# Performance work log

Hardware: AMD Instinct MI355X
Metric: run time of the kernel (lower is better)

Reference implementation:

```python
import jax, jax.numpy as jnp
import numpy as np

B, C, H, W = 128, 512, 8, 64   # batch, featrue_layers, feature-map H/W
HID, EMB = 512, 512            # hidden_dim_de, embedding_size


def setup_inputs() -> dict:
    key = jax.random.key(0)
    ks = jax.random.split(key, 8)
    s_lin = 1.0 / np.sqrt(HID)
    s_conv = 1.0 / np.sqrt(C * 9)
    s_att = 1.0 / np.sqrt(EMB)
    return {
        "conv_f": jax.random.normal(ks[0], (B, C, H, W), jnp.float32),
        "h": jax.random.normal(ks[1], (B, HID), jnp.float32),
        "W_h": jax.random.uniform(ks[2], (EMB, HID), jnp.float32, -s_lin, s_lin),
        "b_h": jax.random.uniform(ks[3], (EMB,), jnp.float32, -s_lin, s_lin),
        "K_conv": jax.random.uniform(ks[4], (EMB, C, 3, 3), jnp.float32, -s_conv, s_conv),
        "b_conv": jax.random.uniform(ks[5], (EMB,), jnp.float32, -s_conv, s_conv),
        "w_att": jax.random.uniform(ks[6], (1, EMB), jnp.float32, -s_att, s_att),
        "b_att": jax.random.uniform(ks[7], (1,), jnp.float32, -s_att, s_att),
    }


def reference(conv_f, h, W_h, b_h, K_conv, b_conv, w_att, b_att):
    b, c, hh, ww = conv_f.shape
    L = hh * ww
    # g_em = Linear(h): [B, EMB], broadcast over L positions
    g_em = h @ W_h.T + b_h                                   # [B, EMB]
    # x_em = Conv2d(conv_f): [B, EMB, H, W] -> [B, L, EMB]
    x_em = jax.lax.conv_general_dilated(
        conv_f, K_conv, window_strides=(1, 1), padding="SAME",
        dimension_numbers=("NCHW", "OIHW", "NCHW"))
    x_em = x_em + b_conv[None, :, None, None]
    x_em = x_em.reshape(b, -1, L).transpose(0, 2, 1)         # [B, L, EMB]
    # additive attention scores (dropout = identity in eval mode)
    feat = jnp.tanh(x_em + g_em[:, None, :])                 # [B, L, EMB]
    e = feat @ w_att[0] + b_att[0]                           # [B, L]
    alpha = jax.nn.softmax(e, axis=-1)                       # [B, L]
    # weighted sum over positions of the ORIGINAL features
    org = conv_f.reshape(b, c, L)                            # [B, C, L]
    att_out = jnp.einsum("bl,bcl->bc", alpha, org)           # [B, C]
    return att_out, alpha
```

## Files before the change

kernel.cpp:

```cpp
#include <hip/hip_runtime.h>
#include <hip/hip_bf16.h>
#include <stdint.h>

#define B_ 128
#define C_ 512
#define H_ 8
#define W_ 64
#define L_ 512
#define EMB_ 512
#define HID_ 512
#define M_ 65536
#define PH 10
#define PW 66
#define PADSZ (B_*PH*PW*C_)
#define BT_SZ (9*EMB_*C_)
#define GEM_SZ (B_*EMB_)

typedef __attribute__((ext_vector_type(8))) short short8;
typedef __attribute__((ext_vector_type(4))) float f32x4;

__device__ __forceinline__ void gload16(const void* g, void* l) {
    __builtin_amdgcn_global_load_lds(
        (const __attribute__((address_space(1))) unsigned int*)g,
        (__attribute__((address_space(3))) unsigned int*)l, 16, 0, 0);
}

__device__ __forceinline__ float fast_tanh(float x) {
    float e = __expf(2.0f * fabsf(x));
    float r = 1.0f - __fdividef(2.0f, e + 1.0f);
    return copysignf(r, x);
}

__global__ __launch_bounds__(256) void k_pad(const float* __restrict__ cf,
                                             __hip_bfloat16* __restrict__ pad) {
    int bid = blockIdx.x, t = threadIdx.x;
    int b = bid >> 3, y = bid & 7;
    for (int cc = 0; cc < 2; ++cc) {
        int c = cc * 256 + t;
        const float* src = cf + ((size_t)(b * C_ + c) * H_ + y) * W_;
        __hip_bfloat16* dst = pad + ((size_t)(b * PH + y + 1) * PW + 1) * C_ + c;
#pragma unroll
        for (int x = 0; x < W_; ++x)
            dst[(size_t)x * C_] = __float2bfloat16(src[x]);
    }
}

__global__ __launch_bounds__(256) void k_wt(const float* __restrict__ kc,
                                            __hip_bfloat16* __restrict__ bt) {
    int e = blockIdx.x, t = threadIdx.x;
    for (int cc = 0; cc < 2; ++cc) {
        int c = cc * 256 + t;
        const float* src = kc + (size_t)(e * C_ + c) * 9;
#pragma unroll
        for (int tap = 0; tap < 9; ++tap)
            bt[(size_t)tap * EMB_ * C_ + e * C_ + c] = __float2bfloat16(src[tap]);
    }
}

__global__ __launch_bounds__(256) void k_gem(const float* __restrict__ h,
                                             const float* __restrict__ Wh,
                                             const float* __restrict__ bh,
                                             float* __restrict__ gem) {
    int b = blockIdx.x, t = threadIdx.x;
    __shared__ float hs[HID_];
    hs[t] = h[b * HID_ + t];
    hs[t + 256] = h[b * HID_ + t + 256];
    __syncthreads();
    for (int e = t; e < EMB_; e += 256) {
        float acc = bh[e];
        const float4* wr = (const float4*)(Wh + (size_t)e * HID_);
#pragma unroll 4
        for (int k4 = 0; k4 < HID_ / 4; ++k4) {
            float4 w = wr[k4];
            const float* hp = &hs[k4 * 4];
            acc += w.x * hp[0] + w.y * hp[1] + w.z * hp[2] + w.w * hp[3];
        }
        gem[b * EMB_ + e] = acc;
    }
}

#define MFMA16(a,b,c) __builtin_amdgcn_mfma_f32_16x16x32_bf16(a,b,c,0,0,0)

__global__ __launch_bounds__(512, 2) void k_conv(const __hip_bfloat16* __restrict__ pad,
                                                 const __hip_bfloat16* __restrict__ bt,
                                                 const float* __restrict__ gem,
                                                 const float* __restrict__ bconv,
                                                 const float* __restrict__ watt,
                                                 float* __restrict__ sp) {
    __shared__ __align__(16) char lds[131072];
    const int tid = threadIdx.x;
    const int lane = tid & 63, wid = tid >> 6;
    const int wm = wid >> 2, wn = wid & 3;
    int bid0 = blockIdx.x;
    int bid = (bid0 & 7) * 64 + (bid0 >> 3);
    const int tile_m = bid >> 1, tile_n = bid & 1;
    const int b = tile_m >> 1;

    int gA[4], gB[4];
#pragma unroll
    for (int i = 0; i < 4; ++i) {
        int s = i * 8192 + tid * 16;
        int row = s >> 7;
        int clocal = ((s & 127) ^ ((row & 7) << 4)) >> 1;
        int m = tile_m * 256 + row;
        int y = (m >> 6) & 7;
        int x = m & 63;
        gA[i] = ((b * PH + y) * PW + x) * C_ + clocal;
        int e = tile_n * 256 + row;
        gB[i] = e * C_ + clocal;
    }
    const int lsw = wid * 1024;

    const int la = lane & 15, lg = lane >> 4;
    const int xorv = (la & 7) << 4;
    const int cb0 = (lg * 16) ^ xorv;
    const int cb1 = (64 + lg * 16) ^ xorv;

    f32x4 acc[8][4];
#pragma unroll
    for (int i = 0; i < 8; ++i)
#pragma unroll
        for (int j = 0; j < 4; ++j) acc[i][j] = (f32x4){0.f, 0.f, 0.f, 0.f};

#define STAGE_A(i, nb, aofs) gload16(pad + gA[i] + (aofs), lds + (nb)*65536 + (i)*8192 + lsw)
#define STAGE_B(i, nb, bofs) gload16(bt + gB[i] + (bofs), lds + (nb)*65536 + 32768 + (i)*8192 + lsw)

    STAGE_A(0, 0, 0); STAGE_A(1, 0, 0); STAGE_A(2, 0, 0); STAGE_A(3, 0, 0);
    STAGE_B(0, 0, 0); STAGE_B(1, 0, 0); STAGE_B(2, 0, 0); STAGE_B(3, 0, 0);

    for (int kt = 0; kt < 72; ++kt) {
        const int cur = kt & 1, nb = cur ^ 1;
        const char* bufA = lds + cur * 65536;
        const char* bufB = bufA + 32768;
        const int ktn = (kt < 71) ? kt + 1 : 71;
        const int tapn = ktn >> 3;
        const int dyn_ = tapn / 3, dxn_ = tapn - dyn_ * 3;
        const int aofsn = (dyn_ * PW + dxn_) * C_ + ((ktn & 7) << 6);
        const int bofsn = tapn * (EMB_ * C_) + ((ktn & 7) << 6);

        short8 af[8], bq0, bq1;
        STAGE_A(0, nb, aofsn); STAGE_A(1, nb, aofsn);
        asm volatile("s_waitcnt vmcnt(2)" ::: "memory");
        __builtin_amdgcn_s_barrier();
#pragma unroll
        for (int fm = 0; fm < 8; ++fm)
            af[fm] = *(const short8*)(bufA + (wm * 128 + fm * 16 + la) * 128 + cb0);
        bq0 = *(const short8*)(bufB + (wn * 64 + la) * 128 + cb0);
        bq1 = *(const short8*)(bufB + (wn * 64 + 16 + la) * 128 + cb0);
        __builtin_amdgcn_s_setprio(1);
#pragma unroll
        for (int fm = 0; fm < 8; ++fm) {
            acc[fm][0] = MFMA16(af[fm], bq0, acc[fm][0]);
            acc[fm][1] = MFMA16(af[fm], bq1, acc[fm][1]);
        }
        __builtin_amdgcn_s_setprio(0);
        STAGE_A(2, nb, aofsn); STAGE_A(3, nb, aofsn);
        bq0 = *(const short8*)(bufB + (wn * 64 + 32 + la) * 128 + cb0);
        bq1 = *(const short8*)(bufB + (wn * 64 + 48 + la) * 128 + cb0);
        __builtin_amdgcn_s_setprio(1);
#pragma unroll
        for (int fm = 0; fm < 8; ++fm) {
            acc[fm][2] = MFMA16(af[fm], bq0, acc[fm][2]);
            acc[fm][3] = MFMA16(af[fm], bq1, acc[fm][3]);
        }
        __builtin_amdgcn_s_setprio(0);
        STAGE_B(0, nb, bofsn); STAGE_B(1, nb, bofsn);
#pragma unroll
        for (int fm = 0; fm < 8; ++fm)
            af[fm] = *(const short8*)(bufA + (wm * 128 + fm * 16 + la) * 128 + cb1);
        bq0 = *(const short8*)(bufB + (wn * 64 + la) * 128 + cb1);
        bq1 = *(const short8*)(bufB + (wn * 64 + 16 + la) * 128 + cb1);
        __builtin_amdgcn_s_setprio(1);
#pragma unroll
        for (int fm = 0; fm < 8; ++fm) {
            acc[fm][0] = MFMA16(af[fm], bq0, acc[fm][0]);
            acc[fm][1] = MFMA16(af[fm], bq1, acc[fm][1]);
        }
        __builtin_amdgcn_s_setprio(0);
        STAGE_B(2, nb, bofsn); STAGE_B(3, nb, bofsn);
        bq0 = *(const short8*)(bufB + (wn * 64 + 32 + la) * 128 + cb1);
        bq1 = *(const short8*)(bufB + (wn * 64 + 48 + la) * 128 + cb1);
        __builtin_amdgcn_s_setprio(1);
#pragma unroll
        for (int fm = 0; fm < 8; ++fm) {
            acc[fm][2] = MFMA16(af[fm], bq0, acc[fm][2]);
            acc[fm][3] = MFMA16(af[fm], bq1, acc[fm][3]);
        }
        __builtin_amdgcn_s_setprio(0);
        __builtin_amdgcn_s_barrier();
    }
    asm volatile("s_waitcnt vmcnt(0)" ::: "memory");

    const int part = tile_n * 4 + wn;
    float addv[4], wv[4];
#pragma unroll
    for (int fn = 0; fn < 4; ++fn) {
        int e = tile_n * 256 + wn * 64 + fn * 16 + la;
        addv[fn] = bconv[e] + gem[b * EMB_ + e];
        wv[fn] = watt[e];
    }
#pragma unroll
    for (int fm = 0; fm < 8; ++fm) {
        float sj[4] = {0.f, 0.f, 0.f, 0.f};
#pragma unroll
        for (int fn = 0; fn < 4; ++fn)
#pragma unroll
            for (int j = 0; j < 4; ++j)
                sj[j] += fast_tanh(acc[fm][fn][j] + addv[fn]) * wv[fn];
#pragma unroll
        for (int mask = 1; mask < 16; mask <<= 1)
#pragma unroll
            for (int j = 0; j < 4; ++j)
                sj[j] += __shfl_xor(sj[j], mask, 64);
        if (la == 0) {
            int mrow = tile_m * 256 + wm * 128 + fm * 16 + lg * 4;
            *(float4*)(sp + (size_t)part * M_ + mrow) =
                make_float4(sj[0], sj[1], sj[2], sj[3]);
        }
    }
}

__global__ __launch_bounds__(512) void k_softmax(const float* __restrict__ sp,
                                                 const float* __restrict__ batt,
                                                 float* __restrict__ alpha) {
    int b = blockIdx.x, t = threadIdx.x;
    float s = batt[0];
#pragma unroll
    for (int p = 0; p < 8; ++p) s += sp[(size_t)p * M_ + b * L_ + t];
    int lane = t & 63, wid = t >> 6;
    __shared__ float red[8];
    float m = s;
#pragma unroll
    for (int mask = 1; mask < 64; mask <<= 1) m = fmaxf(m, __shfl_xor(m, mask, 64));
    if (lane == 0) red[wid] = m;
    __syncthreads();
    float M = red[0];
#pragma unroll
    for (int i = 1; i < 8; ++i) M = fmaxf(M, red[i]);
    float ev = __expf(s - M);
    float sum = ev;
#pragma unroll
    for (int mask = 1; mask < 64; mask <<= 1) sum += __shfl_xor(sum, mask, 64);
    __syncthreads();
    if (lane == 0) red[wid] = sum;
    __syncthreads();
    float S = 0.f;
#pragma unroll
    for (int i = 0; i < 8; ++i) S += red[i];
    alpha[b * L_ + t] = ev / S;
}

__global__ __launch_bounds__(256) void k_att(const float* __restrict__ cf,
                                             const float* __restrict__ alpha,
                                             float* __restrict__ att) {
    int bid = blockIdx.x;
    int b = bid >> 7, cg = bid & 127;
    int t = threadIdx.x, lane = t & 63, wid = t >> 6;
    int c = cg * 4 + wid;
    const float4* xr = (const float4*)(cf + (size_t)(b * C_ + c) * L_);
    const float4* ar = (const float4*)(alpha + b * L_);
    float acc = 0.f;
#pragma unroll
    for (int it = 0; it < 2; ++it) {
        float4 xv = xr[it * 64 + lane];
        float4 av = ar[it * 64 + lane];
        acc += xv.x * av.x + xv.y * av.y + xv.z * av.z + xv.w * av.w;
    }
#pragma unroll
    for (int mask = 1; mask < 64; mask <<= 1) acc += __shfl_xor(acc, mask, 64);
    if (lane == 0) att[b * C_ + c] = acc;
}

extern "C" void kernel_launch(void* const* d_in, const int* in_sizes, int n_in,
                              void* d_out, int out_size, void* d_ws, size_t ws_size,
                              hipStream_t stream) {
    const float* conv_f = (const float*)d_in[0];
    const float* h      = (const float*)d_in[1];
    const float* W_h    = (const float*)d_in[2];
    const float* b_h    = (const float*)d_in[3];
    const float* K_conv = (const float*)d_in[4];
    const float* b_conv = (const float*)d_in[5];
    const float* w_att  = (const float*)d_in[6];
    const float* b_att  = (const float*)d_in[7];
    float* out = (float*)d_out;

    char* ws = (char*)d_ws;
    __hip_bfloat16* pad = (__hip_bfloat16*)ws;
    __hip_bfloat16* bt  = (__hip_bfloat16*)(ws + (size_t)PADSZ * 2);
    float* gem = (float*)(ws + (size_t)PADSZ * 2 + (size_t)BT_SZ * 2);
    float* sp  = gem + GEM_SZ;

    hipMemsetAsync(pad, 0, (size_t)PADSZ * 2, stream);
    k_pad<<<B_ * H_, 256, 0, stream>>>(conv_f, pad);
    k_wt<<<EMB_, 256, 0, stream>>>(K_conv, bt);
    k_gem<<<B_, 256, 0, stream>>>(h, W_h, b_h, gem);
    k_conv<<<512, 512, 0, stream>>>(pad, bt, gem, b_conv, w_att, sp);
    float* alpha = out + B_ * C_;
    k_softmax<<<B_, 512, 0, stream>>>(sp, b_att, alpha);
    k_att<<<B_ * C_ / 4, 256, 0, stream>>>(conv_f, alpha, out);
}
```

Baseline: 527.7 us.

## Switch conv GEMM to 32x32 MFMA, fuse pad zeroing, parallelize gem

The conv GEMM inner loop now uses 32x32x16 bf16 MFMA tiles, which cuts LDS fragment reads per MFMA. All next-tile global-to-LDS loads are issued at the start of each iteration rather than interleaved with compute. The full-buffer memset of the padded input is replaced by zeroing only the border rows and columns inside the pad kernel. The linear-projection kernel is split over 8x more blocks with a 4-way k-split. The risks are reduced overlap of loads with MFMA and more register pressure from the larger accumulators.

```diff
diff --git a/kernel.cpp b/kernel.cpp
--- a/kernel.cpp
+++ b/kernel.cpp
@@ -18,6 +18,7 @@
 
 typedef __attribute__((ext_vector_type(8))) short short8;
 typedef __attribute__((ext_vector_type(4))) float f32x4;
+typedef __attribute__((ext_vector_type(16))) float f32x16;
 
 __device__ __forceinline__ void gload16(const void* g, void* l) {
     __builtin_amdgcn_global_load_lds(
@@ -43,6 +44,19 @@
         for (int x = 0; x < W_; ++x)
             dst[(size_t)x * C_] = __float2bfloat16(src[x]);
     }
+    __hip_bfloat16 z = __float2bfloat16(0.0f);
+    for (int c = t; c < C_; c += 256) {
+        pad[((size_t)(b * PH + y + 1) * PW + 0) * C_ + c] = z;
+        pad[((size_t)(b * PH + y + 1) * PW + 65) * C_ + c] = z;
+    }
+    if (y == 0) {
+        unsigned int* r0 = (unsigned int*)(pad + (size_t)(b * PH + 0) * PW * C_);
+        for (int i = t; i < PW * C_ / 2; i += 256) r0[i] = 0u;
+    }
+    if (y == 7) {
+        unsigned int* r9 = (unsigned int*)(pad + (size_t)(b * PH + 9) * PW * C_);
+        for (int i = t; i < PW * C_ / 2; i += 256) r9[i] = 0u;
+    }
 }
 
 __global__ __launch_bounds__(256) void k_wt(const float* __restrict__ kc,
@@ -61,25 +75,27 @@
                                              const float* __restrict__ Wh,
                                              const float* __restrict__ bh,
                                              float* __restrict__ gem) {
-    int b = blockIdx.x, t = threadIdx.x;
+    int bid = blockIdx.x, t = threadIdx.x;
+    int b = bid >> 3, eg = bid & 7;
     __shared__ float hs[HID_];
     hs[t] = h[b * HID_ + t];
     hs[t + 256] = h[b * HID_ + t + 256];
     __syncthreads();
-    for (int e = t; e < EMB_; e += 256) {
-        float acc = bh[e];
-        const float4* wr = (const float4*)(Wh + (size_t)e * HID_);
-#pragma unroll 4
-        for (int k4 = 0; k4 < HID_ / 4; ++k4) {
-            float4 w = wr[k4];
-            const float* hp = &hs[k4 * 4];
-            acc += w.x * hp[0] + w.y * hp[1] + w.z * hp[2] + w.w * hp[3];
-        }
-        gem[b * EMB_ + e] = acc;
-    }
-}
-
-#define MFMA16(a,b,c) __builtin_amdgcn_mfma_f32_16x16x32_bf16(a,b,c,0,0,0)
+    int e = eg * 64 + (t >> 2), ks = t & 3;
+    const float4* wr = (const float4*)(Wh + (size_t)e * HID_ + ks * 128);
+    const float* hp = &hs[ks * 128];
+    float acc = 0.f;
+#pragma unroll
+    for (int i = 0; i < 32; ++i) {
+        float4 w = wr[i];
+        acc += w.x * hp[i*4] + w.y * hp[i*4+1] + w.z * hp[i*4+2] + w.w * hp[i*4+3];
+    }
+    acc += __shfl_xor(acc, 1, 64);
+    acc += __shfl_xor(acc, 2, 64);
+    if (ks == 0) gem[b * EMB_ + e] = acc + bh[e];
+}
+
+#define MFMA32(a,b,c) __builtin_amdgcn_mfma_f32_32x32x16_bf16(a,b,c,0,0,0)
 
 __global__ __launch_bounds__(512, 2) void k_conv(const __hip_bfloat16* __restrict__ pad,
                                                  const __hip_bfloat16* __restrict__ bt,
@@ -111,16 +127,16 @@
     }
     const int lsw = wid * 1024;
 
-    const int la = lane & 15, lg = lane >> 4;
-    const int xorv = (la & 7) << 4;
-    const int cb0 = (lg * 16) ^ xorv;
-    const int cb1 = (64 + lg * 16) ^ xorv;
-
-    f32x4 acc[8][4];
-#pragma unroll
-    for (int i = 0; i < 8; ++i)
-#pragma unroll
-        for (int j = 0; j < 4; ++j) acc[i][j] = (f32x4){0.f, 0.f, 0.f, 0.f};
+    const int la31 = lane & 31, hh = lane >> 5;
+    const int xorv = (lane & 7) << 4;
+
+    f32x16 acc[4][2];
+#pragma unroll
+    for (int i = 0; i < 4; ++i)
+#pragma unroll
+        for (int j = 0; j < 2; ++j)
+#pragma unroll
+            for (int r = 0; r < 16; ++r) acc[i][j][r] = 0.f;
 
 #define STAGE_A(i, nb, aofs) gload16(pad + gA[i] + (aofs), lds + (nb)*65536 + (i)*8192 + lsw)
 #define STAGE_B(i, nb, bofs) gload16(bt + gB[i] + (bofs), lds + (nb)*65536 + 32768 + (i)*8192 + lsw)
@@ -138,84 +154,66 @@
         const int aofsn = (dyn_ * PW + dxn_) * C_ + ((ktn & 7) << 6);
         const int bofsn = tapn * (EMB_ * C_) + ((ktn & 7) << 6);
 
-        short8 af[8], bq0, bq1;
         STAGE_A(0, nb, aofsn); STAGE_A(1, nb, aofsn);
-        asm volatile("s_waitcnt vmcnt(2)" ::: "memory");
+        STAGE_A(2, nb, aofsn); STAGE_A(3, nb, aofsn);
+        STAGE_B(0, nb, bofsn); STAGE_B(1, nb, bofsn);
+        STAGE_B(2, nb, bofsn); STAGE_B(3, nb, bofsn);
+        asm volatile("s_waitcnt vmcnt(8)" ::: "memory");
         __builtin_amdgcn_s_barrier();
-#pragma unroll
-        for (int fm = 0; fm < 8; ++fm)
-            af[fm] = *(const short8*)(bufA + (wm * 128 + fm * 16 + la) * 128 + cb0);
-        bq0 = *(const short8*)(bufB + (wn * 64 + la) * 128 + cb0);
-        bq1 = *(const short8*)(bufB + (wn * 64 + 16 + la) * 128 + cb0);
-        __builtin_amdgcn_s_setprio(1);
-#pragma unroll
-        for (int fm = 0; fm < 8; ++fm) {
-            acc[fm][0] = MFMA16(af[fm], bq0, acc[fm][0]);
-            acc[fm][1] = MFMA16(af[fm], bq1, acc[fm][1]);
+
+#pragma unroll
+        for (int kk = 0; kk < 4; ++kk) {
+            const int cb = (kk * 32 + hh * 16) ^ xorv;
+            short8 a0 = *(const short8*)(bufA + (wm * 128 +  0 + la31) * 128 + cb);
+            short8 a1 = *(const short8*)(bufA + (wm * 128 + 32 + la31) * 128 + cb);
+            short8 a2 = *(const short8*)(bufA + (wm * 128 + 64 + la31) * 128 + cb);
+            short8 a3 = *(const short8*)(bufA + (wm * 128 + 96 + la31) * 128 + cb);
+            short8 b0 = *(const short8*)(bufB + (wn * 64 +  0 + la31) * 128 + cb);
+            short8 b1 = *(const short8*)(bufB + (wn * 64 + 32 + la31) * 128 + cb);
+            __builtin_amdgcn_s_setprio(1);
+            acc[0][0] = MFMA32(a0, b0, acc[0][0]);
+            acc[0][1] = MFMA32(a0, b1, acc[0][1]);
+            acc[1][0] = MFMA32(a1, b0, acc[1][0]);
+            acc[1][1] = MFMA32(a1, b1, acc[1][1]);
+            acc[2][0] = MFMA32(a2, b0, acc[2][0]);
+            acc[2][1] = MFMA32(a2, b1, acc[2][1]);
+            acc[3][0] = MFMA32(a3, b0, acc[3][0]);
+            acc[3][1] = MFMA32(a3, b1, acc[3][1]);
+            __builtin_amdgcn_s_setprio(0);
         }
-        __builtin_amdgcn_s_setprio(0);
-        STAGE_A(2, nb, aofsn); STAGE_A(3, nb, aofsn);
-        bq0 = *(const short8*)(bufB + (wn * 64 + 32 + la) * 128 + cb0);
-        bq1 = *(const short8*)(bufB + (wn * 64 + 48 + la) * 128 + cb0);
-        __builtin_amdgcn_s_setprio(1);
-#pragma unroll
-        for (int fm = 0; fm < 8; ++fm) {
-            acc[fm][2] = MFMA16(af[fm], bq0, acc[fm][2]);
-            acc[fm][3] = MFMA16(af[fm], bq1, acc[fm][3]);
-        }
-        __builtin_amdgcn_s_setprio(0);
-        STAGE_B(0, nb, bofsn); STAGE_B(1, nb, bofsn);
-#pragma unroll
-        for (int fm = 0; fm < 8; ++fm)
-            af[fm] = *(const short8*)(bufA + (wm * 128 + fm * 16 + la) * 128 + cb1);
-        bq0 = *(const short8*)(bufB + (wn * 64 + la) * 128 + cb1);
-        bq1 = *(const short8*)(bufB + (wn * 64 + 16 + la) * 128 + cb1);
-        __builtin_amdgcn_s_setprio(1);
-#pragma unroll
-        for (int fm = 0; fm < 8; ++fm) {
-            acc[fm][0] = MFMA16(af[fm], bq0, acc[fm][0]);
-            acc[fm][1] = MFMA16(af[fm], bq1, acc[fm][1]);
-        }
-        __builtin_amdgcn_s_setprio(0);
-        STAGE_B(2, nb, bofsn); STAGE_B(3, nb, bofsn);
-        bq0 = *(const short8*)(bufB + (wn * 64 + 32 + la) * 128 + cb1);
-        bq1 = *(const short8*)(bufB + (wn * 64 + 48 + la) * 128 + cb1);
-        __builtin_amdgcn_s_setprio(1);
-#pragma unroll
-        for (int fm = 0; fm < 8; ++fm) {
-            acc[fm][2] = MFMA16(af[fm], bq0, acc[fm][2]);
-            acc[fm][3] = MFMA16(af[fm], bq1, acc[fm][3]);
-        }
-        __builtin_amdgcn_s_setprio(0);
         __builtin_amdgcn_s_barrier();
     }
     asm volatile("s_waitcnt vmcnt(0)" ::: "memory");
 
     const int part = tile_n * 4 + wn;
-    float addv[4], wv[4];
-#pragma unroll
-    for (int fn = 0; fn < 4; ++fn) {
-        int e = tile_n * 256 + wn * 64 + fn * 16 + la;
+    float addv[2], wv[2];
+#pragma unroll
+    for (int fn = 0; fn < 2; ++fn) {
+        int e = tile_n * 256 + wn * 64 + fn * 32 + la31;
         addv[fn] = bconv[e] + gem[b * EMB_ + e];
         wv[fn] = watt[e];
     }
 #pragma unroll
-    for (int fm = 0; fm < 8; ++fm) {
-        float sj[4] = {0.f, 0.f, 0.f, 0.f};
-#pragma unroll
-        for (int fn = 0; fn < 4; ++fn)
-#pragma unroll
-            for (int j = 0; j < 4; ++j)
-                sj[j] += fast_tanh(acc[fm][fn][j] + addv[fn]) * wv[fn];
-#pragma unroll
-        for (int mask = 1; mask < 16; mask <<= 1)
-#pragma unroll
-            for (int j = 0; j < 4; ++j)
-                sj[j] += __shfl_xor(sj[j], mask, 64);
-        if (la == 0) {
-            int mrow = tile_m * 256 + wm * 128 + fm * 16 + lg * 4;
-            *(float4*)(sp + (size_t)part * M_ + mrow) =
-                make_float4(sj[0], sj[1], sj[2], sj[3]);
+    for (int fm = 0; fm < 4; ++fm) {
+        float sj[16];
+#pragma unroll
+        for (int r = 0; r < 16; ++r) sj[r] = 0.f;
+#pragma unroll
+        for (int fn = 0; fn < 2; ++fn)
+#pragma unroll
+            for (int r = 0; r < 16; ++r)
+                sj[r] += fast_tanh(acc[fm][fn][r] + addv[fn]) * wv[fn];
+#pragma unroll
+        for (int mask = 1; mask < 32; mask <<= 1)
+#pragma unroll
+            for (int r = 0; r < 16; ++r)
+                sj[r] += __shfl_xor(sj[r], mask, 64);
+        if (la31 == 0) {
+            int mbase = tile_m * 256 + wm * 128 + fm * 32 + hh * 4;
+#pragma unroll
+            for (int q = 0; q < 4; ++q)
+                *(float4*)(sp + (size_t)part * M_ + mbase + q * 8) =
+                    make_float4(sj[q*4], sj[q*4+1], sj[q*4+2], sj[q*4+3]);
         }
     }
 }
@@ -290,10 +288,9 @@
     float* gem = (float*)(ws + (size_t)PADSZ * 2 + (size_t)BT_SZ * 2);
     float* sp  = gem + GEM_SZ;
 
-    hipMemsetAsync(pad, 0, (size_t)PADSZ * 2, stream);
     k_pad<<<B_ * H_, 256, 0, stream>>>(conv_f, pad);
     k_wt<<<EMB_, 256, 0, stream>>>(K_conv, bt);
-    k_gem<<<B_, 256, 0, stream>>>(h, W_h, b_h, gem);
+    k_gem<<<B_ * 8, 256, 0, stream>>>(h, W_h, b_h, gem);
     k_conv<<<512, 512, 0, stream>>>(pad, bt, gem, b_conv, w_att, sp);
     float* alpha = out + B_ * C_;
     k_softmax<<<B_, 512, 0, stream>>>(sp, b_att, alpha);
```

Result: slower. 546.8 us (+3.6%).
